# Performance work log

Measured on AMD Instinct MI355X. Metric: run time of the kernel, lower is better.

## Reference

```python
import jax, jax.numpy as jnp
import numpy as np

HEATMAPS_LOSS_FACTOR = 1.0
PUSH_LOSS_FACTOR = 0.001
PULL_LOSS_FACTOR = 0.001

B, K, H, W, M = 16, 17, 256, 256, 30  # batch, joints, heatmap HxW, max people
N = K * H * W  # flattened tag length per image


def setup_inputs() -> dict:
    key = jax.random.key(0)
    k1, k2, k3, k4, k5, k6 = jax.random.split(key, 6)
    heatmaps_pred = jax.random.normal(k1, (B, K, H, W), dtype=jnp.float32)
    heatmaps = jax.random.uniform(k2, (B, K, H, W), dtype=jnp.float32)
    masks = (jax.random.uniform(k3, (B, K, H, W)) > 0.1).astype(jnp.float32)
    tags_pred = jax.random.normal(k4, (B, K, H, W), dtype=jnp.float32)
    idx = jax.random.randint(k5, (B, M, K), 0, N)
    vis = jax.random.randint(k6, (B, M, K), 0, 2)  # ~half joints visible
    joints = jnp.stack([idx, vis], axis=-1).astype(jnp.int32)
    return {
        "heatmaps_pred": heatmaps_pred,
        "heatmaps": heatmaps,
        "masks": masks,
        "tags_pred": tags_pred,
        "joints": joints,
    }


def _single_tag_loss(tag_flat, joints_img):
    # tag_flat: [N], joints_img: [M, K, 2] (flat index, visibility)
    idx = joints_img[..., 0]                      # [M, K]
    vis = (joints_img[..., 1] > 0)                # [M, K] bool
    visf = vis.astype(tag_flat.dtype)
    t = tag_flat[idx]                             # [M, K] gathered tags
    cnt = jnp.sum(visf, axis=-1)                  # [M] visible joints per person
    person_valid = cnt > 0                        # [M]
    safe_cnt = jnp.maximum(cnt, 1.0)
    mu = jnp.sum(t * visf, axis=-1) / safe_cnt    # [M] per-person mean tag
    pull_pp = jnp.sum(visf * (t - mu[:, None]) ** 2, axis=-1) / safe_cnt  # [M]
    n = jnp.sum(person_valid.astype(tag_flat.dtype))  # num_tags
    pull = jnp.sum(jnp.where(person_valid, pull_pp, 0.0)) / jnp.maximum(n, 1.0)
    # push: pairwise exp(-(mu_i - mu_j)^2) over valid persons; diagonal sums to n
    diff = mu[:, None] - mu[None, :]              # [M, M]
    pair_mask = person_valid[:, None] & person_valid[None, :]
    s = jnp.sum(jnp.where(pair_mask, jnp.exp(-(diff ** 2)), 0.0))
    denom = jnp.maximum((n - 1.0) * n, 1.0)
    push = jnp.where(n >= 2.0, (s - n) / denom * 0.5, 0.0)
    return push, pull


def reference(heatmaps_pred, heatmaps, masks, tags_pred, joints):
    # HeatmapLoss: mean over all dims of (pred - gt)^2 * mask
    heatmaps_loss = jnp.mean((heatmaps_pred - heatmaps) ** 2 * masks)
    heatmaps_loss = heatmaps_loss * HEATMAPS_LOSS_FACTOR
    # AELoss over flattened tag maps, vectorized across the batch
    b = tags_pred.shape[0]
    tag_flat = tags_pred.reshape(b, -1)           # [B, N]
    push, pull = jax.vmap(_single_tag_loss)(tag_flat, joints)
    push_loss = jnp.mean(push) * PUSH_LOSS_FACTOR
    pull_loss = jnp.mean(pull) * PULL_LOSS_FACTOR
    return (heatmaps_loss, push_loss, pull_loss)
```

## Files before the change

kernel.cpp:

```cpp
#include <hip/hip_runtime.h>

#define Bn 16
#define Kn 17
#define Hn 256
#define Wn 256
#define Mn 30
#define NFLAT (Kn * Hn * Wn)
#define TOTAL ((long long)Bn * Kn * Hn * Wn)
#define NVEC  ((int)(TOTAL / 4))

#define HEAT_BLOCKS 2176
#define THREADS 256
#define GROUPS 2
#define VPG 4
#define AE_BLOCKS Bn
#define NBLOCKS (HEAT_BLOCKS + AE_BLOCKS)
#define TSTRIDE (HEAT_BLOCKS * THREADS)

__global__ __launch_bounds__(THREADS) void fused_kernel(
    const float4* __restrict__ pred,
    const float4* __restrict__ gt,
    const float4* __restrict__ mask,
    const float* __restrict__ tags,
    const int* __restrict__ joints,
    float* __restrict__ partial,
    float* __restrict__ push_arr,
    float* __restrict__ pull_arr) {
    __shared__ float smem[64];

    if (blockIdx.x >= AE_BLOCKS) {
        int hb = blockIdx.x - AE_BLOCKS;
        int t = hb * THREADS + threadIdx.x;
        float acc0 = 0.f, acc1 = 0.f, acc2 = 0.f, acc3 = 0.f;
#pragma unroll
        for (int g = 0; g < GROUPS; ++g) {
            int base = (g * TSTRIDE + t) * VPG;
            float4 p0 = pred[base + 0], p1 = pred[base + 1];
            float4 p2 = pred[base + 2], p3 = pred[base + 3];
            float4 g0 = gt[base + 0],   g1 = gt[base + 1];
            float4 g2 = gt[base + 2],   g3 = gt[base + 3];
            float4 m0 = mask[base + 0], m1 = mask[base + 1];
            float4 m2 = mask[base + 2], m3 = mask[base + 3];
            float dx, dy, dz, dw;
            dx = p0.x - g0.x; dy = p0.y - g0.y; dz = p0.z - g0.z; dw = p0.w - g0.w;
            acc0 += dx * dx * m0.x + dy * dy * m0.y + dz * dz * m0.z + dw * dw * m0.w;
            dx = p1.x - g1.x; dy = p1.y - g1.y; dz = p1.z - g1.z; dw = p1.w - g1.w;
            acc1 += dx * dx * m1.x + dy * dy * m1.y + dz * dz * m1.z + dw * dw * m1.w;
            dx = p2.x - g2.x; dy = p2.y - g2.y; dz = p2.z - g2.z; dw = p2.w - g2.w;
            acc2 += dx * dx * m2.x + dy * dy * m2.y + dz * dz * m2.z + dw * dw * m2.w;
            dx = p3.x - g3.x; dy = p3.y - g3.y; dz = p3.z - g3.z; dw = p3.w - g3.w;
            acc3 += dx * dx * m3.x + dy * dy * m3.y + dz * dz * m3.z + dw * dw * m3.w;
        }
        float a = (acc0 + acc1) + (acc2 + acc3);
        for (int off = 32; off > 0; off >>= 1) a += __shfl_down(a, off, 64);
        int wave = threadIdx.x >> 6;
        if ((threadIdx.x & 63) == 0) smem[wave] = a;
        __syncthreads();
        if (threadIdx.x == 0)
            partial[hb] = smem[0] + smem[1] + smem[2] + smem[3];
    } else {
        int b = blockIdx.x;
        int lane = threadIdx.x;

        float mu = 0.f, pullpp = 0.f, validf = 0.f;
        if (lane < Mn) {
            const int* jb = joints + ((long long)(b * Mn + lane) * Kn) * 2;
            const float* tb = tags + (long long)b * NFLAT;
            float t[Kn], v[Kn];
            float cnt = 0.f, st = 0.f;
#pragma unroll
            for (int k = 0; k < Kn; k++) {
                int id = jb[2 * k];
                int vi = jb[2 * k + 1];
                float tv = tb[id];
                t[k] = tv;
                v[k] = (vi > 0) ? 1.f : 0.f;
                cnt += v[k];
                st += v[k] * tv;
            }
            float sc = fmaxf(cnt, 1.f);
            mu = st / sc;
            float pp = 0.f;
#pragma unroll
            for (int k = 0; k < Kn; k++) {
                float d = t[k] - mu;
                pp += v[k] * d * d;
            }
            pullpp = pp / sc;
            validf = (cnt > 0.f) ? 1.f : 0.f;
            smem[lane] = mu;
            smem[32 + lane] = validf;
        }
        __syncthreads();

        if (lane < 64) {
            float nv = validf;
            float pv = (validf > 0.f) ? pullpp : 0.f;
            float sm = 0.f;
            if (lane < Mn && validf > 0.f) {
                for (int j = 0; j < Mn; j++) {
                    if (smem[32 + j] > 0.f) {
                        float d = mu - smem[j];
                        sm += expf(-(d * d));
                    }
                }
            }
            for (int off = 32; off > 0; off >>= 1) {
                nv += __shfl_down(nv, off, 64);
                pv += __shfl_down(pv, off, 64);
                sm += __shfl_down(sm, off, 64);
            }
            if (lane == 0) {
                float n = nv;
                float pull = pv / fmaxf(n, 1.f);
                float denom = fmaxf((n - 1.f) * n, 1.f);
                float push = (n >= 2.f) ? (sm - n) / denom * 0.5f : 0.f;
                push_arr[b] = push;
                pull_arr[b] = pull;
            }
        }
    }
}

__global__ __launch_bounds__(256) void finalize_kernel(
    const float* __restrict__ partial,
    const float* __restrict__ push_arr,
    const float* __restrict__ pull_arr,
    float* __restrict__ out) {
    __shared__ double sd[256];
    double acc = 0.0;
    for (int i = threadIdx.x; i < HEAT_BLOCKS; i += 256) acc += (double)partial[i];
    sd[threadIdx.x] = acc;
    __syncthreads();
    for (int off = 128; off > 0; off >>= 1) {
        if (threadIdx.x < off) sd[threadIdx.x] += sd[threadIdx.x + off];
        __syncthreads();
    }
    if (threadIdx.x == 0) {
        double heat = sd[0] / (double)TOTAL;
        float psum = 0.f, lsum = 0.f;
        for (int b = 0; b < Bn; b++) {
            psum += push_arr[b];
            lsum += pull_arr[b];
        }
        out[0] = (float)heat;
        out[1] = (psum / (float)Bn) * 0.001f;
        out[2] = (lsum / (float)Bn) * 0.001f;
    }
}

extern "C" void kernel_launch(void* const* d_in, const int* in_sizes, int n_in,
                              void* d_out, int out_size, void* d_ws, size_t ws_size,
                              hipStream_t stream) {
    const float* heatmaps_pred = (const float*)d_in[0];
    const float* heatmaps      = (const float*)d_in[1];
    const float* masks         = (const float*)d_in[2];
    const float* tags_pred     = (const float*)d_in[3];
    const int*   joints        = (const int*)d_in[4];
    float* out = (float*)d_out;

    float* ws = (float*)d_ws;
    float* partial  = ws;
    float* push_arr = ws + HEAT_BLOCKS;
    float* pull_arr = push_arr + Bn;

    fused_kernel<<<NBLOCKS, THREADS, 0, stream>>>(
        (const float4*)heatmaps_pred, (const float4*)heatmaps,
        (const float4*)masks, tags_pred, joints, partial, push_arr, pull_arr);

    finalize_kernel<<<1, 256, 0, stream>>>(partial, push_arr, pull_arr, out);
}
```

Baseline: 41.75 us.

## Use grid-stride coalesced loop with software prefetch and fewer heatmap blocks

Reduces the heatmap-loss grid from 2176 to 1024 blocks, each thread walking 17 grid-strided float4 elements instead of 8 contiguous ones. Loads for the next iteration are issued before computing the current one, with two alternating accumulators. This aims to improve coalescing, cut block scheduling overhead and finalize partials, at the risk of fewer outstanding loads per thread.

```diff
diff --git a/kernel.cpp b/kernel.cpp
--- a/kernel.cpp
+++ b/kernel.cpp
@@ -9,13 +9,12 @@
 #define TOTAL ((long long)Bn * Kn * Hn * Wn)
 #define NVEC  ((int)(TOTAL / 4))
 
-#define HEAT_BLOCKS 2176
+#define HEAT_BLOCKS 1024
 #define THREADS 256
-#define GROUPS 2
-#define VPG 4
+#define ITERS 17
+#define TSTRIDE (HEAT_BLOCKS * THREADS)
 #define AE_BLOCKS Bn
 #define NBLOCKS (HEAT_BLOCKS + AE_BLOCKS)
-#define TSTRIDE (HEAT_BLOCKS * THREADS)
 
 __global__ __launch_bounds__(THREADS) void fused_kernel(
     const float4* __restrict__ pred,
@@ -31,27 +30,30 @@
     if (blockIdx.x >= AE_BLOCKS) {
         int hb = blockIdx.x - AE_BLOCKS;
         int t = hb * THREADS + threadIdx.x;
-        float acc0 = 0.f, acc1 = 0.f, acc2 = 0.f, acc3 = 0.f;
+        const float4* P = pred + t;
+        const float4* G = gt + t;
+        const float4* M = mask + t;
+
+        float acc0 = 0.f, acc1 = 0.f;
+        float4 p = P[0], g = G[0], m = M[0];
 #pragma unroll
-        for (int g = 0; g < GROUPS; ++g) {
-            int base = (g * TSTRIDE + t) * VPG;
-            float4 p0 = pred[base + 0], p1 = pred[base + 1];
-            float4 p2 = pred[base + 2], p3 = pred[base + 3];
-            float4 g0 = gt[base + 0],   g1 = gt[base + 1];
-            float4 g2 = gt[base + 2],   g3 = gt[base + 3];
-            float4 m0 = mask[base + 0], m1 = mask[base + 1];
-            float4 m2 = mask[base + 2], m3 = mask[base + 3];
-            float dx, dy, dz, dw;
-            dx = p0.x - g0.x; dy = p0.y - g0.y; dz = p0.z - g0.z; dw = p0.w - g0.w;
-            acc0 += dx * dx * m0.x + dy * dy * m0.y + dz * dz * m0.z + dw * dw * m0.w;
-            dx = p1.x - g1.x; dy = p1.y - g1.y; dz = p1.z - g1.z; dw = p1.w - g1.w;
-            acc1 += dx * dx * m1.x + dy * dy * m1.y + dz * dz * m1.z + dw * dw * m1.w;
-            dx = p2.x - g2.x; dy = p2.y - g2.y; dz = p2.z - g2.z; dw = p2.w - g2.w;
-            acc2 += dx * dx * m2.x + dy * dy * m2.y + dz * dz * m2.z + dw * dw * m2.w;
-            dx = p3.x - g3.x; dy = p3.y - g3.y; dz = p3.z - g3.z; dw = p3.w - g3.w;
-            acc3 += dx * dx * m3.x + dy * dy * m3.y + dz * dz * m3.z + dw * dw * m3.w;
+        for (int it = 0; it < ITERS - 1; ++it) {
+            int nx = (it + 1) * TSTRIDE;
+            float4 pn = P[nx];
+            float4 gn = G[nx];
+            float4 mn = M[nx];
+            float dx = p.x - g.x, dy = p.y - g.y, dz = p.z - g.z, dw = p.w - g.w;
+            if (it & 1)
+                acc1 += dx * dx * m.x + dy * dy * m.y + dz * dz * m.z + dw * dw * m.w;
+            else
+                acc0 += dx * dx * m.x + dy * dy * m.y + dz * dz * m.z + dw * dw * m.w;
+            p = pn; g = gn; m = mn;
         }
-        float a = (acc0 + acc1) + (acc2 + acc3);
+        {
+            float dx = p.x - g.x, dy = p.y - g.y, dz = p.z - g.z, dw = p.w - g.w;
+            acc0 += dx * dx * m.x + dy * dy * m.y + dz * dz * m.z + dw * dw * m.w;
+        }
+        float a = acc0 + acc1;
         for (int off = 32; off > 0; off >>= 1) a += __shfl_down(a, off, 64);
         int wave = threadIdx.x >> 6;
         if ((threadIdx.x & 63) == 0) smem[wave] = a;
```

New measurement: 42.17 us. No clear change (+1.0%).
